# Performance work log

Hardware: AMD Instinct MI355X
Metric: run time of the kernel (lower is better)

## Reference

```python
import jax, jax.numpy as jnp
import numpy as np

EPS = 1e-5
KH = KW = 3
PAD = 1

def conv3x3(x, w, b=None):
    out = jax.lax.conv_general_dilated(
        x, w, window_strides=(1, 1), padding=((PAD, PAD), (PAD, PAD)),
        dimension_numbers=("NCHW", "OIHW", "NCHW"))
    if b is not None:
        out = out + b[None, :, None, None]
    return out

def batchnorm(x, gamma, beta):
    # training-mode BatchNorm2d: batch statistics over (N, H, W)
    mean = x.mean(axis=(0, 2, 3), keepdims=True)
    var = x.var(axis=(0, 2, 3), keepdims=True)
    return gamma[None, :, None, None] * (x - mean) / jnp.sqrt(var + EPS) + beta[None, :, None, None]

def bilinear_gather(x, y_pos, x_pos):
    # x: [B,C,H,W]; y_pos/x_pos: [B,P,H,W] (P = KH*KW sampling taps)
    # zero padding outside image (mmcv modulated deform conv semantics)
    B, C, H, W = x.shape
    P = y_pos.shape[1]
    x_flat = x.reshape(B, C, H * W)
    y0 = jnp.floor(y_pos)
    x0 = jnp.floor(x_pos)
    ly = y_pos - y0
    lx = x_pos - x0
    out = jnp.zeros((B, C, P, H, W), dtype=x.dtype)
    for dy, dx, wgt in ((0, 0, (1 - ly) * (1 - lx)), (0, 1, (1 - ly) * lx),
                        (1, 0, ly * (1 - lx)), (1, 1, ly * lx)):
        yi = y0 + dy
        xi = x0 + dx
        valid = ((yi >= 0) & (yi <= H - 1) & (xi >= 0) & (xi <= W - 1)).astype(x.dtype)
        yc = jnp.clip(yi, 0, H - 1).astype(jnp.int32)
        xc = jnp.clip(xi, 0, W - 1).astype(jnp.int32)
        idx = (yc * W + xc).reshape(B, 1, P * H * W)
        vals = jnp.take_along_axis(x_flat, jnp.broadcast_to(idx, (B, C, P * H * W)), axis=2)
        vals = vals.reshape(B, C, P, H, W)
        out = out + vals * (wgt * valid)[:, None]
    return out  # [B,C,P,H,W]

def modulated_deform_conv(x, w_off, b_off, w_dcn):
    B, C, H, W = x.shape
    P = KH * KW
    off = conv3x3(x, w_off, b_off)  # [B, 3*P, H, W]
    o1, o2, m = jnp.split(off, 3, axis=1)
    offset = jnp.concatenate([o1, o2], axis=1)            # [B, 2P, H, W]
    offset = offset.reshape(B, P, 2, H, W)                # channel 2p -> dy, 2p+1 -> dx
    mask = jax.nn.sigmoid(m)                              # [B, P, H, W]
    hh = jnp.arange(H, dtype=x.dtype)
    ww = jnp.arange(W, dtype=x.dtype)
    ky = jnp.arange(KH, dtype=x.dtype)
    kx = jnp.arange(KW, dtype=x.dtype)
    # base sampling grid per tap p = ky*KW + kx: (h - PAD + ky, w - PAD + kx)
    base_y = (hh[None, :] - PAD + ky[:, None])            # [KH, H]
    base_x = (ww[None, :] - PAD + kx[:, None])            # [KW, W]
    base_y = jnp.broadcast_to(base_y[:, None, :, None], (KH, KW, H, W)).reshape(P, H, W)
    base_x = jnp.broadcast_to(base_x[None, :, None, :], (KH, KW, H, W)).reshape(P, H, W)
    y_pos = base_y[None] + offset[:, :, 0]                # [B,P,H,W]
    x_pos = base_x[None] + offset[:, :, 1]
    sampled = bilinear_gather(x, y_pos, x_pos)            # [B,C,P,H,W]
    sampled = sampled * mask[:, None]
    w = w_dcn.reshape(w_dcn.shape[0], C, P)               # [O, C, P]
    return jnp.einsum("bcphw,ocp->bohw", sampled, w)

def setup_inputs() -> dict:
    key = jax.random.key(0)
    ks = jax.random.split(key, 10)
    B, Ch, H, W = 4, 256, 64, 64
    Cin, Cout = 2 * Ch, 256
    P = KH * KW
    inp = {
        "input_v": jax.random.normal(ks[0], (B, Ch, H, W), jnp.float32),
        "input_i": jax.random.normal(ks[1], (B, Ch, H, W), jnp.float32),
        "w_off": jax.random.normal(ks[2], (3 * P, Cin, KH, KW), jnp.float32) * 0.01,
        "b_off": jnp.zeros((3 * P,), jnp.float32),
        "w_dcn": jax.random.normal(ks[3], (Cout, Cin, KH, KW), jnp.float32) * (1.0 / np.sqrt(Cin * P)),
        "gamma1": jnp.ones((Cout,), jnp.float32),
        "beta1": jnp.zeros((Cout,), jnp.float32),
        "w2": jax.random.normal(ks[4], (Cout, Cout, KH, KW), jnp.float32) * (1.0 / np.sqrt(Cout * P)),
        "gamma2": jnp.ones((Cout,), jnp.float32),
        "beta2": jnp.zeros((Cout,), jnp.float32),
    }
    return inp

def reference(input_v, input_i, w_off, b_off, w_dcn, gamma1, beta1, w2, gamma2, beta2):
    x = jnp.concatenate([input_v, input_i], axis=1)
    out = modulated_deform_conv(x, w_off, b_off, w_dcn)
    out = jax.nn.relu(batchnorm(out, gamma1, beta1))
    out = jax.nn.relu(batchnorm(conv3x3(out, w2), gamma2, beta2))
    return out
```

## Files before the change

kernel.cpp:

```cpp
#include <hip/hip_runtime.h>
#include <cstdint>
#include <cstddef>

typedef unsigned short u16;
typedef __attribute__((ext_vector_type(8))) short s16x8;
typedef __attribute__((ext_vector_type(4))) float f32x4;

#define DEV __device__ __forceinline__

DEV float bf2f(short u){
  union { unsigned int i; float f; } v;
  v.i = ((unsigned int)(u16)u) << 16;
  return v.f;
}
DEV short f2bf(float f){
  union { float f; unsigned int i; } v; v.f = f;
  unsigned int u = v.i;
  u += 0x7fffu + ((u >> 16) & 1u);
  return (short)(u >> 16);
}
DEV s16x8 s16x8_zero(){
  s16x8 z;
#pragma unroll
  for(int j=0;j<8;j++) z[j]=0;
  return z;
}
DEV f32x4 f32x4_zero(){
  f32x4 z;
#pragma unroll
  for(int j=0;j<4;j++) z[j]=0.f;
  return z;
}
DEV f32x4 mfma16(s16x8 a, s16x8 b, f32x4 c){
  return __builtin_amdgcn_mfma_f32_16x16x32_bf16(a, b, c, 0, 0, 0);
}
DEV void bar_lds(){
  asm volatile("s_waitcnt lgkmcnt(0)");
  __builtin_amdgcn_s_barrier();
}

static constexpr size_t OFF_ACC_B  = 0;
static constexpr size_t OUT1_ACC_B = 2097152;
static constexpr size_t OUT2_ACC_B = OUT1_ACC_B + 16777216;
static constexpr size_t STATS_B    = OUT2_ACC_B + 16777216;
static constexpr size_t ZERO_BYTES = STATS_B + 4096;
static constexpr size_t XN_B       = ZERO_BYTES;
static constexpr size_t OUT1N_B    = XN_B + 16777216;
static constexpr size_t WOFFT_B    = OUT1N_B + 8388608;
static constexpr size_t WDCNT_B    = WOFFT_B + 294912;
static constexpr size_t W2T_B      = WDCNT_B + 2359296;

__global__ void k_x_to_nhwc(const float* __restrict__ v, const float* __restrict__ vi,
                            u16* __restrict__ xn){
  __shared__ float tile[64][65];
  const int b = blockIdx.z, c0 = blockIdx.y*64, hw0 = blockIdx.x*64;
  const float* src = (c0 < 256) ? (v  + ((size_t)b*256 + c0)      *4096)
                                : (vi + ((size_t)b*256 + (c0-256))*4096);
  const int t = threadIdx.x;
#pragma unroll
  for(int k=0;k<16;k++){
    int idx = t + k*256;
    int cl = idx >> 6, wl = idx & 63;
    tile[cl][wl] = src[(size_t)cl*4096 + hw0 + wl];
  }
  __syncthreads();
#pragma unroll
  for(int k=0;k<16;k++){
    int idx = t + k*256;
    int wl = idx >> 6, cl = idx & 63;
    xn[(size_t)(b*4096 + hw0 + wl)*512 + c0 + cl] = (u16)f2bf(tile[cl][wl]);
  }
}

__global__ void k_prep_woff(const float* __restrict__ w, u16* __restrict__ wt){
  int idx = blockIdx.x*256 + threadIdx.x;
  if(idx >= 32*4608) return;
  int n = idx / 4608, k = idx % 4608;
  int t = k >> 9, c = k & 511;
  float val = (n < 27) ? w[(size_t)(n*512 + c)*9 + t] : 0.f;
  wt[idx] = (u16)f2bf(val);
}
__global__ void k_prep_wdcn(const float* __restrict__ w, u16* __restrict__ wt){
  int idx = blockIdx.x*256 + threadIdx.x;
  if(idx >= 256*4608) return;
  int n = idx / 4608, k = idx % 4608;
  int t = k >> 9, c = k & 511;
  wt[idx] = (u16)f2bf(w[(size_t)(n*512 + c)*9 + t]);
}
__global__ void k_prep_w2(const float* __restrict__ w, u16* __restrict__ wt){
  int idx = blockIdx.x*256 + threadIdx.x;
  if(idx >= 256*2304) return;
  int n = idx / 2304, k = idx % 2304;
  int t = k >> 8, c = k & 255;
  wt[idx] = (u16)f2bf(w[(size_t)(n*256 + c)*9 + t]);
}

__global__ __launch_bounds__(256, 2) void k_conv_off(
    const u16* __restrict__ xn, const u16* __restrict__ wt, float* __restrict__ offa){
  __shared__ short A_lds[4][128][8];
  __shared__ short B_lds[4][32][8];
  const int tid = threadIdx.x;
  const int lane = tid & 63, wid = tid >> 6;
  const int quad = lane >> 4, ln = lane & 15;
  const int m0 = blockIdx.x * 128;
  const int b = m0 >> 12;
  const int h0 = (m0 & 4095) >> 6;
  const int ks = blockIdx.y;
  const int ts0 = (ks == 3) ? 6 : ks*2;
  const int ntap = (ks == 3) ? 3 : 2;
  const int m_base = wid * 32;
  const int r = tid >> 1, sp = (tid & 1) * 2;
  const int h_r = h0 + (r >> 6), w_r = r & 63;
  const s16x8* Ap = (const s16x8*)A_lds;
  const s16x8* Bp = (const s16x8*)B_lds;
  f32x4 acc[2][2];
#pragma unroll
  for(int mf=0;mf<2;mf++)
#pragma unroll
    for(int nf=0;nf<2;nf++) acc[mf][nf] = f32x4_zero();

  auto load_it = [&](int it, s16x8& v0, s16x8& v1, s16x8& bv){
    const int tp = ts0 + (it >> 4);
    const int cA = (it & 15)*32;
    const int ty = tp/3, tx = tp - ty*3;
    const int y = h_r - 1 + ty, x = w_r - 1 + tx;
    const bool vld = (y>=0) & (y<64) & (x>=0) & (x<64);
    v0 = s16x8_zero(); v1 = s16x8_zero();
    if(vld){
      const u16* src = xn + ((size_t)((b<<12) + (y<<6) + x) << 9) + cA + sp*8;
      v0 = *(const s16x8*)(src);
      v1 = *(const s16x8*)(src + 8);
    }
    if(tid < 128){
      const int n = tid & 31, s2 = tid >> 5;
      bv = *(const s16x8*)(wt + (size_t)n*4608 + tp*512 + cA + s2*8);
    }
  };

  const int NIT = ntap * 16;
  s16x8 v0a, v1a, bva, v0b, v1b, bvb;
  bva = s16x8_zero(); bvb = s16x8_zero();
  load_it(0, v0a, v1a, bva);
  load_it(1, v0b, v1b, bvb);
  for(int it = 0; it < NIT; it += 2){
    bar_lds();
    *(s16x8*)(&A_lds[sp][r][0])   = v0a;
    *(s16x8*)(&A_lds[sp+1][r][0]) = v1a;
    if(tid < 128){
      const int n = tid & 31, s2 = tid >> 5;
      *(s16x8*)(&B_lds[s2][n][0]) = bva;
    }
    if(it + 2 < NIT) load_it(it + 2, v0a, v1a, bva);
    bar_lds();
    {
      s16x8 a0 = Ap[quad*128 + m_base + ln];
      s16x8 a1 = Ap[quad*128 + m_base + 16 + ln];
      s16x8 b0 = Bp[quad*32 + ln];
      s16x8 b1 = Bp[quad*32 + 16 + ln];
      acc[0][0] = mfma16(a0, b0, acc[0][0]);
      acc[0][1] = mfma16(a0, b1, acc[0][1]);
      acc[1][0] = mfma16(a1, b0, acc[1][0]);
      acc[1][1] = mfma16(a1, b1, acc[1][1]);
    }
    bar_lds();
    *(s16x8*)(&A_lds[sp][r][0])   = v0b;
    *(s16x8*)(&A_lds[sp+1][r][0]) = v1b;
    if(tid < 128){
      const int n = tid & 31, s2 = tid >> 5;
      *(s16x8*)(&B_lds[s2][n][0]) = bvb;
    }
    if(it + 3 < NIT) load_it(it + 3, v0b, v1b, bvb);
    bar_lds();
    {
      s16x8 a0 = Ap[quad*128 + m_base + ln];
      s16x8 a1 = Ap[quad*128 + m_base + 16 + ln];
      s16x8 b0 = Bp[quad*32 + ln];
      s16x8 b1 = Bp[quad*32 + 16 + ln];
      acc[0][0] = mfma16(a0, b0, acc[0][0]);
      acc[0][1] = mfma16(a0, b1, acc[0][1]);
      acc[1][0] = mfma16(a1, b0, acc[1][0]);
      acc[1][1] = mfma16(a1, b1, acc[1][1]);
    }
  }
#pragma unroll
  for(int mf=0;mf<2;mf++)
#pragma unroll
    for(int nf=0;nf<2;nf++){
      const int col = nf*16 + ln;
#pragma unroll
      for(int i=0;i<4;i++){
        const int row = m_base + mf*16 + quad*4 + i;
        unsafeAtomicAdd(offa + (size_t)(m0+row)*32 + col, acc[mf][nf][i]);
      }
    }
}

__global__ __launch_bounds__(256, 2) void k_dcn(
    const u16* __restrict__ xn, const u16* __restrict__ wt,
    const float* __restrict__ offa, const float* __restrict__ boff,
    float* __restrict__ outa){
  __shared__ short A_lds[4][64][8];
  __shared__ short B_lds[4][256][8];
  __shared__ int   p_ofs[5][4][64];
  __shared__ float p_wgt[5][4][64];
  const int tid = threadIdx.x;
  const int lane = tid & 63, wid = tid >> 6;
  const int quad = lane >> 4, ln = lane & 15;
  const int m0 = blockIdx.x * 64;
  const int b = m0 >> 12;
  const int h = (m0 & 4095) >> 6;
  const int tg = blockIdx.y;
  const int ts0 = tg ? 4 : 0;
  const int ntap = tg ? 5 : 4;
  const int wm = wid >> 1, wn = wid & 1;
  const int m_base = wm*32, n_base = wn*128;
  const int r = tid >> 2, sub = tid & 3;
  const s16x8* Ap = (const s16x8*)A_lds;
  const s16x8* Bp = (const s16x8*)B_lds;
  const u16* wrowt = wt + (size_t)tid*4608;
  f32x4 acc[2][8];
#pragma unroll
  for(int mf=0;mf<2;mf++)
#pragma unroll
    for(int nf=0;nf<8;nf++) acc[mf][nf] = f32x4_zero();

  {
    const int rr = tid & 63;
    const float* orow = offa + (size_t)(m0+rr)*32;
    for(int tpi = tid >> 6; tpi < ntap; tpi += 4){
      const int tp = ts0 + tpi;
      float dy = orow[2*tp]   + boff[2*tp];
      float dx = orow[2*tp+1] + boff[2*tp+1];
      float mz = orow[18+tp]  + boff[18+tp];
      float mk = 1.f / (1.f + expf(-mz));
      float ypos = (float)(h - 1 + tp/3) + dy;
      float xpos = (float)(rr - 1 + tp%3) + dx;
      float y0f = floorf(ypos), x0f = floorf(xpos);
      float ly = ypos - y0f, lx = xpos - x0f;
      int y0 = (int)y0f, x0 = (int)x0f;
#pragma unroll
      for(int k=0;k<4;k++){
        int ddy = k >> 1, ddx = k & 1;
        int yi = y0 + ddy, xi = x0 + ddx;
        bool vv = (yi >= 0) & (yi < 64) & (xi >= 0) & (xi < 64);
        float wk = (ddy ? ly : 1.f-ly) * (ddx ? lx : 1.f-lx) * mk;
        if(!vv) wk = 0.f;
        int yc = yi < 0 ? 0 : (yi > 63 ? 63 : yi);
        int xc = xi < 0 ? 0 : (xi > 63 ? 63 : xi);
        p_ofs[tpi][k][rr] = ((b << 12) + (yc << 6) + xc) << 9;
        p_wgt[tpi][k][rr] = wk;
      }
    }
  }
  __syncthreads();

  auto loadA = [&](int it, s16x8& a0, s16x8& a1, s16x8& a2, s16x8& a3,
                   float& w0, float& w1, float& w2, float& w3){
    const int tpi = it >> 4;
    const int c0 = (it & 15)*32 + sub*8;
    w0 = p_wgt[tpi][0][r]; w1 = p_wgt[tpi][1][r];
    w2 = p_wgt[tpi][2][r]; w3 = p_wgt[tpi][3][r];
    a0 = *(const s16x8*)(xn + p_ofs[tpi][0][r] + c0);
    a1 = *(const s16x8*)(xn + p_ofs[tpi][1][r] + c0);
    a2 = *(const s16x8*)(xn + p_ofs[tpi][2][r] + c0);
    a3 = *(const s16x8*)(xn + p_ofs[tpi][3][r] + c0);
  };
  auto loadB = [&](int it, s16x8& b0, s16x8& b1, s16x8& b2, s16x8& b3){
    const int kb = (ts0 + (it >> 4))*512 + (it & 15)*32;
    b0 = *(const s16x8*)(wrowt + kb);
    b1 = *(const s16x8*)(wrowt + kb + 8);
    b2 = *(const s16x8*)(wrowt + kb + 16);
    b3 = *(const s16x8*)(wrowt + kb + 24);
  };
  auto blend = [&](const s16x8& a0, const s16x8& a1, const s16x8& a2, const s16x8& a3,
                   float w0, float w1, float w2, float w3){
    s16x8 pk;
#pragma unroll
    for(int j=0;j<8;j++){
      float f = w0 * bf2f(a0[j]);
      f = fmaf(w1, bf2f(a1[j]), f);
      f = fmaf(w2, bf2f(a2[j]), f);
      f = fmaf(w3, bf2f(a3[j]), f);
      pk[j] = f2bf(f);
    }
    return pk;
  };

  const int NIT = ntap * 16;
  s16x8 aA0,aA1,aA2,aA3, bA0,bA1,bA2,bA3;
  s16x8 aB0,aB1,aB2,aB3, bB0,bB1,bB2,bB3;
  float wA0,wA1,wA2,wA3, wB0,wB1,wB2,wB3;
  loadA(0, aA0,aA1,aA2,aA3, wA0,wA1,wA2,wA3);
  loadB(0, bA0,bA1,bA2,bA3);
  loadA(1, aB0,aB1,aB2,aB3, wB0,wB1,wB2,wB3);
  loadB(1, bB0,bB1,bB2,bB3);

  for(int it = 0; it < NIT; it += 2){
    {
      s16x8 pk = blend(aA0,aA1,aA2,aA3, wA0,wA1,wA2,wA3);
      if(it + 2 < NIT) loadA(it + 2, aA0,aA1,aA2,aA3, wA0,wA1,wA2,wA3);
      bar_lds();
      *(s16x8*)(&A_lds[sub][r][0]) = pk;
      *(s16x8*)(&B_lds[0][tid][0]) = bA0;
      *(s16x8*)(&B_lds[1][tid][0]) = bA1;
      *(s16x8*)(&B_lds[2][tid][0]) = bA2;
      *(s16x8*)(&B_lds[3][tid][0]) = bA3;
      if(it + 2 < NIT) loadB(it + 2, bA0,bA1,bA2,bA3);
      bar_lds();
      s16x8 af0 = Ap[quad*64 + m_base + ln];
      s16x8 af1 = Ap[quad*64 + m_base + 16 + ln];
      s16x8 bfr[8];
#pragma unroll
      for(int nf=0;nf<8;nf++) bfr[nf] = Bp[quad*256 + n_base + nf*16 + ln];
#pragma unroll
      for(int nf=0;nf<8;nf++){
        acc[0][nf] = mfma16(af0, bfr[nf], acc[0][nf]);
        acc[1][nf] = mfma16(af1, bfr[nf], acc[1][nf]);
      }
    }
    {
      s16x8 pk = blend(aB0,aB1,aB2,aB3, wB0,wB1,wB2,wB3);
      if(it + 3 < NIT) loadA(it + 3, aB0,aB1,aB2,aB3, wB0,wB1,wB2,wB3);
      bar_lds();
      *(s16x8*)(&A_lds[sub][r][0]) = pk;
      *(s16x8*)(&B_lds[0][tid][0]) = bB0;
      *(s16x8*)(&B_lds[1][tid][0]) = bB1;
      *(s16x8*)(&B_lds[2][tid][0]) = bB2;
      *(s16x8*)(&B_lds[3][tid][0]) = bB3;
      if(it + 3 < NIT) loadB(it + 3, bB0,bB1,bB2,bB3);
      bar_lds();
      s16x8 af0 = Ap[quad*64 + m_base + ln];
      s16x8 af1 = Ap[quad*64 + m_base + 16 + ln];
      s16x8 bfr[8];
#pragma unroll
      for(int nf=0;nf<8;nf++) bfr[nf] = Bp[quad*256 + n_base + nf*16 + ln];
#pragma unroll
      for(int nf=0;nf<8;nf++){
        acc[0][nf] = mfma16(af0, bfr[nf], acc[0][nf]);
        acc[1][nf] = mfma16(af1, bfr[nf], acc[1][nf]);
      }
    }
  }
#pragma unroll
  for(int mf=0;mf<2;mf++)
#pragma unroll
    for(int nf=0;nf<8;nf++){
      const int col = n_base + nf*16 + ln;
#pragma unroll
      for(int i=0;i<4;i++){
        const int row = m_base + mf*16 + quad*4 + i;
        unsafeAtomicAdd(outa + (size_t)(m0+row)*256 + col, acc[mf][nf][i]);
      }
    }
}

__global__ __launch_bounds__(256, 2) void k_conv2(
    const u16* __restrict__ a_in, const u16* __restrict__ wt, float* __restrict__ outa){
  __shared__ short A_lds[4][64][8];
  __shared__ short B_lds[4][256][8];
  const int tid = threadIdx.x;
  const int lane = tid & 63, wid = tid >> 6;
  const int quad = lane >> 4, ln = lane & 15;
  const int m0 = blockIdx.x * 64;
  const int b = m0 >> 12;
  const int h = (m0 & 4095) >> 6;
  const int tg = blockIdx.y;
  const int ts0 = tg ? 4 : 0;
  const int ntap = tg ? 5 : 4;
  const int wm = wid >> 1, wn = wid & 1;
  const int m_base = wm*32, n_base = wn*128;
  const int r = tid >> 2, sub = tid & 3;
  const s16x8* Ap = (const s16x8*)A_lds;
  const s16x8* Bp = (const s16x8*)B_lds;
  const u16* wrowt = wt + (size_t)tid*2304;
  f32x4 acc[2][8];
#pragma unroll
  for(int mf=0;mf<2;mf++)
#pragma unroll
    for(int nf=0;nf<8;nf++) acc[mf][nf] = f32x4_zero();

  auto load_it = [&](int it, s16x8& va, s16x8& b0, s16x8& b1, s16x8& b2, s16x8& b3){
    const int tp = ts0 + (it >> 3);
    const int c0 = (it & 7)*32;
    const int ty = tp/3, tx = tp - ty*3;
    const int y = h - 1 + ty, x = r - 1 + tx;
    const bool vld = (y>=0) & (y<64) & (x>=0) & (x<64);
    va = s16x8_zero();
    if(vld) va = *(const s16x8*)(a_in + (((size_t)((b<<12) + (y<<6) + x)) << 8) + c0 + sub*8);
    const int kb = tp*256 + c0;
    b0 = *(const s16x8*)(wrowt + kb);
    b1 = *(const s16x8*)(wrowt + kb + 8);
    b2 = *(const s16x8*)(wrowt + kb + 16);
    b3 = *(const s16x8*)(wrowt + kb + 24);
  };

  const int NIT = ntap * 8;
  s16x8 vA, bA0,bA1,bA2,bA3;
  s16x8 vB, bB0,bB1,bB2,bB3;
  load_it(0, vA, bA0,bA1,bA2,bA3);
  load_it(1, vB, bB0,bB1,bB2,bB3);
  for(int it = 0; it < NIT; it += 2){
    bar_lds();
    *(s16x8*)(&A_lds[sub][r][0]) = vA;
    *(s16x8*)(&B_lds[0][tid][0]) = bA0;
    *(s16x8*)(&B_lds[1][tid][0]) = bA1;
    *(s16x8*)(&B_lds[2][tid][0]) = bA2;
    *(s16x8*)(&B_lds[3][tid][0]) = bA3;
    if(it + 2 < NIT) load_it(it + 2, vA, bA0,bA1,bA2,bA3);
    bar_lds();
    {
      s16x8 af0 = Ap[quad*64 + m_base + ln];
      s16x8 af1 = Ap[quad*64 + m_base + 16 + ln];
      s16x8 bfr[8];
#pragma unroll
      for(int nf=0;nf<8;nf++) bfr[nf] = Bp[quad*256 + n_base + nf*16 + ln];
#pragma unroll
      for(int nf=0;nf<8;nf++){
        acc[0][nf] = mfma16(af0, bfr[nf], acc[0][nf]);
        acc[1][nf] = mfma16(af1, bfr[nf], acc[1][nf]);
      }
    }
    bar_lds();
    *(s16x8*)(&A_lds[sub][r][0]) = vB;
    *(s16x8*)(&B_lds[0][tid][0]) = bB0;
    *(s16x8*)(&B_lds[1][tid][0]) = bB1;
    *(s16x8*)(&B_lds[2][tid][0]) = bB2;
    *(s16x8*)(&B_lds[3][tid][0]) = bB3;
    if(it + 3 < NIT) load_it(it + 3, vB, bB0,bB1,bB2,bB3);
    bar_lds();
    {
      s16x8 af0 = Ap[quad*64 + m_base + ln];
      s16x8 af1 = Ap[quad*64 + m_base + 16 + ln];
      s16x8 bfr[8];
#pragma unroll
      for(int nf=0;nf<8;nf++) bfr[nf] = Bp[quad*256 + n_base + nf*16 + ln];
#pragma unroll
      for(int nf=0;nf<8;nf++){
        acc[0][nf] = mfma16(af0, bfr[nf], acc[0][nf]);
        acc[1][nf] = mfma16(af1, bfr[nf], acc[1][nf]);
      }
    }
  }
#pragma unroll
  for(int mf=0;mf<2;mf++)
#pragma unroll
    for(int nf=0;nf<8;nf++){
      const int col = n_base + nf*16 + ln;
#pragma unroll
      for(int i=0;i<4;i++){
        const int row = m_base + mf*16 + quad*4 + i;
        unsafeAtomicAdd(outa + (size_t)(m0+row)*256 + col, acc[mf][nf][i]);
      }
    }
}

__global__ void k_stats(const float* __restrict__ acc, float* __restrict__ sum,
                        float* __restrict__ sq){
  const int m0 = blockIdx.x*64;
  const int c = threadIdx.x;
  float s = 0.f, q = 0.f;
  for(int i=0;i<64;i++){
    float v = acc[(size_t)(m0+i)*256 + c];
    s += v; q += v*v;
  }
  unsafeAtomicAdd(sum + c, s);
  unsafeAtomicAdd(sq + c, q);
}

__global__ void k_bn1(const float* __restrict__ acc, const float* __restrict__ sum,
                      const float* __restrict__ sq, const float* __restrict__ g,
                      const float* __restrict__ bt, u16* __restrict__ o){
  __shared__ float sc[256], sh[256];
  const int t = threadIdx.x;
  {
    float mean = sum[t] * (1.f/16384.f);
    float var  = sq[t] * (1.f/16384.f) - mean*mean;
    float rstd = rsqrtf(var + 1e-5f);
    float s = g[t] * rstd;
    sc[t] = s; sh[t] = bt[t] - mean*s;
  }
  __syncthreads();
  const int c4 = (t & 63) * 4;
  const float s0 = sc[c4], s1 = sc[c4+1], s2 = sc[c4+2], s3 = sc[c4+3];
  const float h0 = sh[c4], h1 = sh[c4+1], h2 = sh[c4+2], h3 = sh[c4+3];
#pragma unroll
  for(int k=0;k<4;k++){
    int m = blockIdx.x*16 + k*4 + (t>>6);
    const float4 v = *(const float4*)(acc + (size_t)m*256 + c4);
    unsigned int lo = (unsigned int)(u16)f2bf(fmaxf(0.f, v.x*s0 + h0))
                    | ((unsigned int)(u16)f2bf(fmaxf(0.f, v.y*s1 + h1)) << 16);
    unsigned int hi = (unsigned int)(u16)f2bf(fmaxf(0.f, v.z*s2 + h2))
                    | ((unsigned int)(u16)f2bf(fmaxf(0.f, v.w*s3 + h3)) << 16);
    uint2 pr; pr.x = lo; pr.y = hi;
    *(uint2*)(o + (size_t)m*256 + c4) = pr;
  }
}

__global__ void k_bn2_out(const float* __restrict__ acc, const float* __restrict__ sum,
                          const float* __restrict__ sq, const float* __restrict__ g,
                          const float* __restrict__ bt, float* __restrict__ out){
  __shared__ float tile[64][65];
  __shared__ float sc[64], sh[64];
  const int t = threadIdx.x;
  const int b = blockIdx.z, c0 = blockIdx.y*64, hw0 = blockIdx.x*64;
  if(t < 64){
    int c = c0 + t;
    float mean = sum[c] * (1.f/16384.f);
    float var  = sq[c] * (1.f/16384.f) - mean*mean;
    float rstd = rsqrtf(var + 1e-5f);
    float s = g[c] * rstd;
    sc[t] = s; sh[t] = bt[c] - mean*s;
  }
  __syncthreads();
#pragma unroll
  for(int k=0;k<16;k++){
    int idx = t + k*256;
    int wl = idx >> 6, cl = idx & 63;
    float v = acc[(size_t)((b<<12) + hw0 + wl)*256 + c0 + cl];
    tile[wl][cl] = fmaxf(0.f, v*sc[cl] + sh[cl]);
  }
  __syncthreads();
#pragma unroll
  for(int k=0;k<16;k++){
    int idx = t + k*256;
    int cl = idx >> 6, wl = idx & 63;
    out[(size_t)(b*256 + c0 + cl)*4096 + hw0 + wl] = tile[wl][cl];
  }
}

extern "C" void kernel_launch(void* const* d_in, const int* in_sizes, int n_in,
                              void* d_out, int out_size, void* d_ws, size_t ws_size,
                              hipStream_t stream){
  const float* in_v  = (const float*)d_in[0];
  const float* in_i  = (const float*)d_in[1];
  const float* w_off = (const float*)d_in[2];
  const float* b_off = (const float*)d_in[3];
  const float* w_dcn = (const float*)d_in[4];
  const float* g1    = (const float*)d_in[5];
  const float* bt1   = (const float*)d_in[6];
  const float* w2    = (const float*)d_in[7];
  const float* g2    = (const float*)d_in[8];
  const float* bt2   = (const float*)d_in[9];
  float* out = (float*)d_out;
  char* ws = (char*)d_ws;

  float* off_acc  = (float*)(ws + OFF_ACC_B);
  float* out1_acc = (float*)(ws + OUT1_ACC_B);
  float* out2_acc = (float*)(ws + OUT2_ACC_B);
  float* stats    = (float*)(ws + STATS_B);
  float* sum1 = stats,       *sq1 = stats + 256;
  float* sum2 = stats + 512, *sq2 = stats + 768;
  u16* xn    = (u16*)(ws + XN_B);
  u16* out1n = (u16*)(ws + OUT1N_B);
  u16* wofft = (u16*)(ws + WOFFT_B);
  u16* wdcnt = (u16*)(ws + WDCNT_B);
  u16* w2t   = (u16*)(ws + W2T_B);

  hipMemsetAsync(ws, 0, ZERO_BYTES, stream);
  k_x_to_nhwc<<<dim3(64,8,4), 256, 0, stream>>>(in_v, in_i, xn);
  k_prep_woff<<<576, 256, 0, stream>>>(w_off, wofft);
  k_prep_wdcn<<<4608, 256, 0, stream>>>(w_dcn, wdcnt);
  k_prep_w2<<<2304, 256, 0, stream>>>(w2, w2t);
  k_conv_off<<<dim3(128,4), 256, 0, stream>>>(xn, wofft, off_acc);
  k_dcn<<<dim3(256,2), 256, 0, stream>>>(xn, wdcnt, off_acc, b_off, out1_acc);
  k_stats<<<256, 256, 0, stream>>>(out1_acc, sum1, sq1);
  k_bn1<<<1024, 256, 0, stream>>>(out1_acc, sum1, sq1, g1, bt1, out1n);
  k_conv2<<<dim3(256,2), 256, 0, stream>>>(out1n, w2t, out2_acc);
  k_stats<<<256, 256, 0, stream>>>(out2_acc, sum2, sq2);
  k_bn2_out<<<dim3(64,4,4), 256, 0, stream>>>(out2_acc, sum2, sq2, g2, bt2, out);
}
```

Measured before the change: 352.0 us.

## Restructure DCN and conv2 GEMMs with async LDS weight loads and double buffering

Both the deformable-conv GEMM and the second 3x3 conv move from two 256-thread blocks per row tile (split over taps, combined with atomics) to one 512-thread block that covers all taps and writes its output with plain stores. Weights are staged straight into double-buffered LDS with global_load_lds, and the A operand is gathered two steps ahead. Each step now does K=64 with only one barrier. The workspace is reordered so that memset no longer clears the big output accumulators. The cost is half as many blocks (256), one block per CU, and vmcnt waits tuned by hand whose correctness depends on load counts.

After: 367.9 us. 4.5% more time.

```diff
diff --git a/kernel.cpp b/kernel.cpp
--- a/kernel.cpp
+++ b/kernel.cpp
@@ -38,13 +38,20 @@
   asm volatile("s_waitcnt lgkmcnt(0)");
   __builtin_amdgcn_s_barrier();
 }
+DEV void wait_vm4(){ asm volatile("s_waitcnt vmcnt(4)" ::: "memory"); }
+DEV void wait_vm1(){ asm volatile("s_waitcnt vmcnt(1)" ::: "memory"); }
+DEV void gload16(const u16* g, u16* l){
+  __builtin_amdgcn_global_load_lds(
+      (const __attribute__((address_space(1))) unsigned int*)g,
+      (__attribute__((address_space(3))) unsigned int*)l, 16, 0, 0);
+}
 
 static constexpr size_t OFF_ACC_B  = 0;
-static constexpr size_t OUT1_ACC_B = 2097152;
+static constexpr size_t STATS_B    = 2097152;
+static constexpr size_t ZERO_BYTES = STATS_B + 4096;
+static constexpr size_t OUT1_ACC_B = ZERO_BYTES;
 static constexpr size_t OUT2_ACC_B = OUT1_ACC_B + 16777216;
-static constexpr size_t STATS_B    = OUT2_ACC_B + 16777216;
-static constexpr size_t ZERO_BYTES = STATS_B + 4096;
-static constexpr size_t XN_B       = ZERO_BYTES;
+static constexpr size_t XN_B       = OUT2_ACC_B + 16777216;
 static constexpr size_t OUT1N_B    = XN_B + 16777216;
 static constexpr size_t WOFFT_B    = OUT1N_B + 8388608;
 static constexpr size_t WDCNT_B    = WOFFT_B + 294912;
@@ -195,40 +202,33 @@
     }
 }
 
-__global__ __launch_bounds__(256, 2) void k_dcn(
+__global__ __launch_bounds__(512, 1) void k_dcn(
     const u16* __restrict__ xn, const u16* __restrict__ wt,
     const float* __restrict__ offa, const float* __restrict__ boff,
     float* __restrict__ outa){
-  __shared__ short A_lds[4][64][8];
-  __shared__ short B_lds[4][256][8];
-  __shared__ int   p_ofs[5][4][64];
-  __shared__ float p_wgt[5][4][64];
+  __shared__ short A_lds[2][8][64][8];
+  __shared__ short B_lds[2][8][256][8];
+  __shared__ int   p_ofs[9][4][64];
+  __shared__ float p_wgt[9][4][64];
   const int tid = threadIdx.x;
   const int lane = tid & 63, wid = tid >> 6;
   const int quad = lane >> 4, ln = lane & 15;
+  const int wm = wid >> 2, wn = wid & 3;
   const int m0 = blockIdx.x * 64;
   const int b = m0 >> 12;
   const int h = (m0 & 4095) >> 6;
-  const int tg = blockIdx.y;
-  const int ts0 = tg ? 4 : 0;
-  const int ntap = tg ? 5 : 4;
-  const int wm = wid >> 1, wn = wid & 1;
-  const int m_base = wm*32, n_base = wn*128;
-  const int r = tid >> 2, sub = tid & 3;
-  const s16x8* Ap = (const s16x8*)A_lds;
-  const s16x8* Bp = (const s16x8*)B_lds;
-  const u16* wrowt = wt + (size_t)tid*4608;
-  f32x4 acc[2][8];
+  const int r_s = tid >> 3, sub = tid & 7;
+  constexpr int NP = 72;
+  f32x4 acc[2][4];
 #pragma unroll
   for(int mf=0;mf<2;mf++)
 #pragma unroll
-    for(int nf=0;nf<8;nf++) acc[mf][nf] = f32x4_zero();
+    for(int nf=0;nf<4;nf++) acc[mf][nf] = f32x4_zero();
 
   {
     const int rr = tid & 63;
     const float* orow = offa + (size_t)(m0+rr)*32;
-    for(int tpi = tid >> 6; tpi < ntap; tpi += 4){
-      const int tp = ts0 + tpi;
+    for(int tp = tid >> 6; tp < 9; tp += 8){
       float dy = orow[2*tp]   + boff[2*tp];
       float dx = orow[2*tp+1] + boff[2*tp+1];
       float mz = orow[18+tp]  + boff[18+tp];
@@ -247,209 +247,190 @@
         if(!vv) wk = 0.f;
         int yc = yi < 0 ? 0 : (yi > 63 ? 63 : yi);
         int xc = xi < 0 ? 0 : (xi > 63 ? 63 : xi);
-        p_ofs[tpi][k][rr] = ((b << 12) + (yc << 6) + xc) << 9;
-        p_wgt[tpi][k][rr] = wk;
+        p_ofs[tp][k][rr] = ((b << 12) + (yc << 6) + xc) << 9;
+        p_wgt[tp][k][rr] = wk;
       }
     }
   }
   __syncthreads();
 
-  auto loadA = [&](int it, s16x8& a0, s16x8& a1, s16x8& a2, s16x8& a3,
-                   float& w0, float& w1, float& w2, float& w3){
-    const int tpi = it >> 4;
-    const int c0 = (it & 15)*32 + sub*8;
-    w0 = p_wgt[tpi][0][r]; w1 = p_wgt[tpi][1][r];
-    w2 = p_wgt[tpi][2][r]; w3 = p_wgt[tpi][3][r];
-    a0 = *(const s16x8*)(xn + p_ofs[tpi][0][r] + c0);
-    a1 = *(const s16x8*)(xn + p_ofs[tpi][1][r] + c0);
-    a2 = *(const s16x8*)(xn + p_ofs[tpi][2][r] + c0);
-    a3 = *(const s16x8*)(xn + p_ofs[tpi][3][r] + c0);
-  };
-  auto loadB = [&](int it, s16x8& b0, s16x8& b1, s16x8& b2, s16x8& b3){
-    const int kb = (ts0 + (it >> 4))*512 + (it & 15)*32;
-    b0 = *(const s16x8*)(wrowt + kb);
-    b1 = *(const s16x8*)(wrowt + kb + 8);
-    b2 = *(const s16x8*)(wrowt + kb + 16);
-    b3 = *(const s16x8*)(wrowt + kb + 24);
-  };
-  auto blend = [&](const s16x8& a0, const s16x8& a1, const s16x8& a2, const s16x8& a3,
-                   float w0, float w1, float w2, float w3){
+  auto gather = [&](int t, s16x8* g){
+    const int tp = t >> 3;
+    const int kcc = (t & 7)*64 + sub*8;
+#pragma unroll
+    for(int k=0;k<4;k++)
+      g[k] = *(const s16x8*)(xn + p_ofs[tp][k][r_s] + kcc);
+  };
+  auto blendw = [&](int t, const s16x8* g){
+    const int tp = t >> 3;
+    const float w0 = p_wgt[tp][0][r_s], w1 = p_wgt[tp][1][r_s];
+    const float w2 = p_wgt[tp][2][r_s], w3 = p_wgt[tp][3][r_s];
     s16x8 pk;
 #pragma unroll
     for(int j=0;j<8;j++){
-      float f = w0 * bf2f(a0[j]);
-      f = fmaf(w1, bf2f(a1[j]), f);
-      f = fmaf(w2, bf2f(a2[j]), f);
-      f = fmaf(w3, bf2f(a3[j]), f);
+      float f = w0 * bf2f(g[0][j]);
+      f = fmaf(w1, bf2f(g[1][j]), f);
+      f = fmaf(w2, bf2f(g[2][j]), f);
+      f = fmaf(w3, bf2f(g[3][j]), f);
       pk[j] = f2bf(f);
     }
     return pk;
   };
-
-  const int NIT = ntap * 16;
-  s16x8 aA0,aA1,aA2,aA3, bA0,bA1,bA2,bA3;
-  s16x8 aB0,aB1,aB2,aB3, bB0,bB1,bB2,bB3;
-  float wA0,wA1,wA2,wA3, wB0,wB1,wB2,wB3;
-  loadA(0, aA0,aA1,aA2,aA3, wA0,wA1,wA2,wA3);
-  loadB(0, bA0,bA1,bA2,bA3);
-  loadA(1, aB0,aB1,aB2,aB3, wB0,wB1,wB2,wB3);
-  loadB(1, bB0,bB1,bB2,bB3);
-
-  for(int it = 0; it < NIT; it += 2){
-    {
-      s16x8 pk = blend(aA0,aA1,aA2,aA3, wA0,wA1,wA2,wA3);
-      if(it + 2 < NIT) loadA(it + 2, aA0,aA1,aA2,aA3, wA0,wA1,wA2,wA3);
-      bar_lds();
-      *(s16x8*)(&A_lds[sub][r][0]) = pk;
-      *(s16x8*)(&B_lds[0][tid][0]) = bA0;
-      *(s16x8*)(&B_lds[1][tid][0]) = bA1;
-      *(s16x8*)(&B_lds[2][tid][0]) = bA2;
-      *(s16x8*)(&B_lds[3][tid][0]) = bA3;
-      if(it + 2 < NIT) loadB(it + 2, bA0,bA1,bA2,bA3);
-      bar_lds();
-      s16x8 af0 = Ap[quad*64 + m_base + ln];
-      s16x8 af1 = Ap[quad*64 + m_base + 16 + ln];
-      s16x8 bfr[8];
-#pragma unroll
-      for(int nf=0;nf<8;nf++) bfr[nf] = Bp[quad*256 + n_base + nf*16 + ln];
-#pragma unroll
-      for(int nf=0;nf<8;nf++){
-        acc[0][nf] = mfma16(af0, bfr[nf], acc[0][nf]);
-        acc[1][nf] = mfma16(af1, bfr[nf], acc[1][nf]);
+  auto stageB = [&](int t, int bi){
+    const int tp = t >> 3, kc = (t & 7)*64;
+#pragma unroll
+    for(int i=0;i<4;i++){
+      const int li = wid*4 + i;
+      const int sl = li >> 2, n0 = (li & 3)*64;
+      gload16(wt + (size_t)(n0 + lane)*4608 + tp*512 + kc + sl*8,
+              (u16*)&B_lds[bi][sl][n0][0]);
+    }
+  };
+  auto phase = [&](int t, int cur, const s16x8* gB, s16x8* gF){
+    const int nxt = cur ^ 1;
+    if(t + 1 < NP){
+      s16x8 pk = blendw(t + 1, gB);
+      *(s16x8*)&A_lds[nxt][sub][r_s][0] = pk;
+      stageB(t + 1, nxt);
+    }
+    __builtin_amdgcn_sched_barrier(0);
+    if(t + 2 < NP) gather(t + 2, gF);
+#pragma unroll
+    for(int kk=0;kk<2;kk++){
+      s16x8 af0 = *(const s16x8*)&A_lds[cur][kk*4+quad][wm*32 + ln][0];
+      s16x8 af1 = *(const s16x8*)&A_lds[cur][kk*4+quad][wm*32 + 16 + ln][0];
+      s16x8 bf[4];
+#pragma unroll
+      for(int nf=0;nf<4;nf++)
+        bf[nf] = *(const s16x8*)&B_lds[cur][kk*4+quad][wn*64 + nf*16 + ln][0];
+#pragma unroll
+      for(int nf=0;nf<4;nf++){
+        acc[0][nf] = mfma16(af0, bf[nf], acc[0][nf]);
+        acc[1][nf] = mfma16(af1, bf[nf], acc[1][nf]);
       }
     }
-    {
-      s16x8 pk = blend(aB0,aB1,aB2,aB3, wB0,wB1,wB2,wB3);
-      if(it + 3 < NIT) loadA(it + 3, aB0,aB1,aB2,aB3, wB0,wB1,wB2,wB3);
-      bar_lds();
-      *(s16x8*)(&A_lds[sub][r][0]) = pk;
-      *(s16x8*)(&B_lds[0][tid][0]) = bB0;
-      *(s16x8*)(&B_lds[1][tid][0]) = bB1;
-      *(s16x8*)(&B_lds[2][tid][0]) = bB2;
-      *(s16x8*)(&B_lds[3][tid][0]) = bB3;
-      if(it + 3 < NIT) loadB(it + 3, bB0,bB1,bB2,bB3);
-      bar_lds();
-      s16x8 af0 = Ap[quad*64 + m_base + ln];
-      s16x8 af1 = Ap[quad*64 + m_base + 16 + ln];
-      s16x8 bfr[8];
-#pragma unroll
-      for(int nf=0;nf<8;nf++) bfr[nf] = Bp[quad*256 + n_base + nf*16 + ln];
-#pragma unroll
-      for(int nf=0;nf<8;nf++){
-        acc[0][nf] = mfma16(af0, bfr[nf], acc[0][nf]);
-        acc[1][nf] = mfma16(af1, bfr[nf], acc[1][nf]);
+    wait_vm4();
+    bar_lds();
+  };
+
+  s16x8 S0[4], S1[4];
+  gather(0, S0);
+  stageB(0, 0);
+  __builtin_amdgcn_sched_barrier(0);
+  gather(1, S1);
+  {
+    s16x8 pk = blendw(0, S0);
+    *(s16x8*)&A_lds[0][sub][r_s][0] = pk;
+  }
+  wait_vm4();
+  bar_lds();
+
+  for(int t = 0; t < NP; t += 2){
+    phase(t,     0, S1, S0);
+    phase(t + 1, 1, S0, S1);
+  }
+
+#pragma unroll
+  for(int mf=0;mf<2;mf++)
+#pragma unroll
+    for(int nf=0;nf<4;nf++){
+      const int col = wn*64 + nf*16 + ln;
+#pragma unroll
+      for(int i=0;i<4;i++){
+        const int row = m0 + wm*32 + mf*16 + quad*4 + i;
+        outa[(size_t)row*256 + col] = acc[mf][nf][i];
       }
     }
-  }
-#pragma unroll
-  for(int mf=0;mf<2;mf++)
-#pragma unroll
-    for(int nf=0;nf<8;nf++){
-      const int col = n_base + nf*16 + ln;
-#pragma unroll
-      for(int i=0;i<4;i++){
-        const int row = m_base + mf*16 + quad*4 + i;
-        unsafeAtomicAdd(outa + (size_t)(m0+row)*256 + col, acc[mf][nf][i]);
-      }
-    }
-}
-
-__global__ __launch_bounds__(256, 2) void k_conv2(
+}
+
+__global__ __launch_bounds__(512, 1) void k_conv2(
     const u16* __restrict__ a_in, const u16* __restrict__ wt, float* __restrict__ outa){
-  __shared__ short A_lds[4][64][8];
-  __shared__ short B_lds[4][256][8];
+  __shared__ short A_lds[2][8][64][8];
+  __shared__ short B_lds[2][8][256][8];
   const int tid = threadIdx.x;
   const int lane = tid & 63, wid = tid >> 6;
   const int quad = lane >> 4, ln = lane & 15;
+  const int wm = wid >> 2, wn = wid & 3;
   const int m0 = blockIdx.x * 64;
   const int b = m0 >> 12;
   const int h = (m0 & 4095) >> 6;
-  const int tg = blockIdx.y;
-  const int ts0 = tg ? 4 : 0;
-  const int ntap = tg ? 5 : 4;
-  const int wm = wid >> 1, wn = wid & 1;
-  const int m_base = wm*32, n_base = wn*128;
-  const int r = tid >> 2, sub = tid & 3;
-  const s16x8* Ap = (const s16x8*)A_lds;
-  const s16x8* Bp = (const s16x8*)B_lds;
-  const u16* wrowt = wt + (size_t)tid*2304;
-  f32x4 acc[2][8];
+  const int r_s = tid >> 3, sub = tid & 7;
+  constexpr int NP = 36;
+  f32x4 acc[2][4];
 #pragma unroll
   for(int mf=0;mf<2;mf++)
 #pragma unroll
-    for(int nf=0;nf<8;nf++) acc[mf][nf] = f32x4_zero();
-
-  auto load_it = [&](int it, s16x8& va, s16x8& b0, s16x8& b1, s16x8& b2, s16x8& b3){
-    const int tp = ts0 + (it >> 3);
-    const int c0 = (it & 7)*32;
+    for(int nf=0;nf<4;nf++) acc[mf][nf] = f32x4_zero();
+
+  auto loadA = [&](int t, s16x8& va){
+    const int tp = t >> 2;
     const int ty = tp/3, tx = tp - ty*3;
-    const int y = h - 1 + ty, x = r - 1 + tx;
+    const int y = h - 1 + ty, x = r_s - 1 + tx;
     const bool vld = (y>=0) & (y<64) & (x>=0) & (x<64);
     va = s16x8_zero();
-    if(vld) va = *(const s16x8*)(a_in + (((size_t)((b<<12) + (y<<6) + x)) << 8) + c0 + sub*8);
-    const int kb = tp*256 + c0;
-    b0 = *(const s16x8*)(wrowt + kb);
-    b1 = *(const s16x8*)(wrowt + kb + 8);
-    b2 = *(const s16x8*)(wrowt + kb + 16);
-    b3 = *(const s16x8*)(wrowt + kb + 24);
-  };
-
-  const int NIT = ntap * 8;
-  s16x8 vA, bA0,bA1,bA2,bA3;
-  s16x8 vB, bB0,bB1,bB2,bB3;
-  load_it(0, vA, bA0,bA1,bA2,bA3);
-  load_it(1, vB, bB0,bB1,bB2,bB3);
-  for(int it = 0; it < NIT; it += 2){
+    if(vld)
+      va = *(const s16x8*)(a_in + (((size_t)((b<<12) + (y<<6) + x)) << 8)
+                           + (t & 3)*64 + sub*8);
+  };
+  auto stageB = [&](int t, int bi){
+    const int tp = t >> 2, kc = (t & 3)*64;
+#pragma unroll
+    for(int i=0;i<4;i++){
+      const int li = wid*4 + i;
+      const int sl = li >> 2, n0 = (li & 3)*64;
+      gload16(wt + (size_t)(n0 + lane)*2304 + tp*256 + kc + sl*8,
+              (u16*)&B_lds[bi][sl][n0][0]);
+    }
+  };
+  auto phase = [&](int t, int cur, const s16x8& vB, s16x8& vF){
+    const int nxt = cur ^ 1;
+    if(t + 1 < NP){
+      *(s16x8*)&A_lds[nxt][sub][r_s][0] = vB;
+      stageB(t + 1, nxt);
+    }
+    __builtin_amdgcn_sched_barrier(0);
+    if(t + 2 < NP) loadA(t + 2, vF);
+#pragma unroll
+    for(int kk=0;kk<2;kk++){
+      s16x8 af0 = *(const s16x8*)&A_lds[cur][kk*4+quad][wm*32 + ln][0];
+      s16x8 af1 = *(const s16x8*)&A_lds[cur][kk*4+quad][wm*32 + 16 + ln][0];
+      s16x8 bf[4];
+#pragma unroll
+      for(int nf=0;nf<4;nf++)
+        bf[nf] = *(const s16x8*)&B_lds[cur][kk*4+quad][wn*64 + nf*16 + ln][0];
+#pragma unroll
+      for(int nf=0;nf<4;nf++){
+        acc[0][nf] = mfma16(af0, bf[nf], acc[0][nf]);
+        acc[1][nf] = mfma16(af1, bf[nf], acc[1][nf]);
+      }
+    }
+    wait_vm1();
     bar_lds();
-    *(s16x8*)(&A_lds[sub][r][0]) = vA;
-    *(s16x8*)(&B_lds[0][tid][0]) = bA0;
-    *(s16x8*)(&B_lds[1][tid][0]) = bA1;
-    *(s16x8*)(&B_lds[2][tid][0]) = bA2;
-    *(s16x8*)(&B_lds[3][tid][0]) = bA3;
-    if(it + 2 < NIT) load_it(it + 2, vA, bA0,bA1,bA2,bA3);
-    bar_lds();
-    {
-      s16x8 af0 = Ap[quad*64 + m_base + ln];
-      s16x8 af1 = Ap[quad*64 + m_base + 16 + ln];
-      s16x8 bfr[8];
-#pragma unroll
-      for(int nf=0;nf<8;nf++) bfr[nf] = Bp[quad*256 + n_base + nf*16 + ln];
-#pragma unroll
-      for(int nf=0;nf<8;nf++){
-        acc[0][nf] = mfma16(af0, bfr[nf], acc[0][nf]);
-        acc[1][nf] = mfma16(af1, bfr[nf], acc[1][nf]);
-      }
-    }
-    bar_lds();
-    *(s16x8*)(&A_lds[sub][r][0]) = vB;
-    *(s16x8*)(&B_lds[0][tid][0]) = bB0;
-    *(s16x8*)(&B_lds[1][tid][0]) = bB1;
-    *(s16x8*)(&B_lds[2][tid][0]) = bB2;
-    *(s16x8*)(&B_lds[3][tid][0]) = bB3;
-    if(it + 3 < NIT) load_it(it + 3, vB, bB0,bB1,bB2,bB3);
-    bar_lds();
-    {
-      s16x8 af0 = Ap[quad*64 + m_base + ln];
-      s16x8 af1 = Ap[quad*64 + m_base + 16 + ln];
-      s16x8 bfr[8];
-#pragma unroll
-      for(int nf=0;nf<8;nf++) bfr[nf] = Bp[quad*256 + n_base + nf*16 + ln];
-#pragma unroll
-      for(int nf=0;nf<8;nf++){
-        acc[0][nf] = mfma16(af0, bfr[nf], acc[0][nf]);
-        acc[1][nf] = mfma16(af1, bfr[nf], acc[1][nf]);
-      }
-    }
-  }
+  };
+
+  s16x8 S0, S1;
+  loadA(0, S0);
+  stageB(0, 0);
+  __builtin_amdgcn_sched_barrier(0);
+  loadA(1, S1);
+  *(s16x8*)&A_lds[0][sub][r_s][0] = S0;
+  wait_vm1();
+  bar_lds();
+
+  for(int t = 0; t < NP; t += 2){
+    phase(t,     0, S1, S0);
+    phase(t + 1, 1, S0, S1);
+  }
+
 #pragma unroll
   for(int mf=0;mf<2;mf++)
 #pragma unroll
-    for(int nf=0;nf<8;nf++){
-      const int col = n_base + nf*16 + ln;
+    for(int nf=0;nf<4;nf++){
+      const int col = wn*64 + nf*16 + ln;
 #pragma unroll
       for(int i=0;i<4;i++){
-        const int row = m_base + mf*16 + quad*4 + i;
-        unsafeAtomicAdd(outa + (size_t)(m0+row)*256 + col, acc[mf][nf][i]);
+        const int row = m0 + wm*32 + mf*16 + quad*4 + i;
+        outa[(size_t)row*256 + col] = acc[mf][nf][i];
       }
     }
 }
@@ -545,9 +526,9 @@
   char* ws = (char*)d_ws;
 
   float* off_acc  = (float*)(ws + OFF_ACC_B);
+  float* stats    = (float*)(ws + STATS_B);
   float* out1_acc = (float*)(ws + OUT1_ACC_B);
   float* out2_acc = (float*)(ws + OUT2_ACC_B);
-  float* stats    = (float*)(ws + STATS_B);
   float* sum1 = stats,       *sq1 = stats + 256;
   float* sum2 = stats + 512, *sq2 = stats + 768;
   u16* xn    = (u16*)(ws + XN_B);
@@ -562,10 +543,10 @@
   k_prep_wdcn<<<4608, 256, 0, stream>>>(w_dcn, wdcnt);
   k_prep_w2<<<2304, 256, 0, stream>>>(w2, w2t);
   k_conv_off<<<dim3(128,4), 256, 0, stream>>>(xn, wofft, off_acc);
-  k_dcn<<<dim3(256,2), 256, 0, stream>>>(xn, wdcnt, off_acc, b_off, out1_acc);
+  k_dcn<<<256, 512, 0, stream>>>(xn, wdcnt, off_acc, b_off, out1_acc);
   k_stats<<<256, 256, 0, stream>>>(out1_acc, sum1, sq1);
   k_bn1<<<1024, 256, 0, stream>>>(out1_acc, sum1, sq1, g1, bt1, out1n);
-  k_conv2<<<dim3(256,2), 256, 0, stream>>>(out1n, w2t, out2_acc);
+  k_conv2<<<256, 512, 0, stream>>>(out1n, w2t, out2_acc);
   k_stats<<<256, 256, 0, stream>>>(out2_acc, sum2, sq2);
   k_bn2_out<<<dim3(64,4,4), 256, 0, stream>>>(out2_acc, sum2, sq2, g2, bt2, out);
 }
```
